# Kernel optimization log

Hardware: AMD Instinct MI355X
Metric: run time of the kernel (lower is better)

## Reference

```python
import jax, jax.numpy as jnp
from jax import lax
import numpy as np


def _conv1d(x, w, b):
    # x: (N, C, L), w: (O, I, K), stride 2, padding 1 -> matches nn.Conv1d(k=4, s=2, p=1)
    y = lax.conv_general_dilated(x, w, window_strides=(2,), padding=[(1, 1)],
                                 dimension_numbers=('NCH', 'OIH', 'NCH'))
    return y + b[None, :, None]


def setup_inputs() -> dict:
    key = jax.random.key(0)
    k = jax.random.split(key, 6)
    B, C_in, T = 32, 256, 2048
    H, D, K_codes = 1024, 512, 1024
    s = 0.02
    return {
        'x': jax.random.normal(k[0], (B, C_in, T), dtype=jnp.float32),
        'w1': jax.random.normal(k[1], (H, C_in, 4), dtype=jnp.float32) * s,
        'b1': jnp.zeros((H,), dtype=jnp.float32),
        'w2': jax.random.normal(k[2], (D, H, 4), dtype=jnp.float32) * s,
        'b2': jnp.zeros((D,), dtype=jnp.float32),
        'codebook': jax.random.normal(k[3], (K_codes, D), dtype=jnp.float32) * s,
    }


def reference(x, w1, b1, w2, b2, codebook):
    z_e = _conv1d(jax.nn.relu(_conv1d(x, w1, b1)), w2, b2)  # (B, D, T/4)
    B, D, T = z_e.shape
    flat = z_e.transpose(0, 2, 1).reshape(-1, D)  # (B*T, D)
    # squared Euclidean distance; argmin identical to cdist(p=2) argmin
    d2 = (jnp.sum(flat * flat, axis=1, keepdims=True)
          - 2.0 * flat @ codebook.T
          + jnp.sum(codebook * codebook, axis=1)[None, :])  # (B*T, K)
    encoding_indices = jnp.argmin(d2, axis=1)  # (B*T,)
    # NOTE: faithful to the original .view(z_e.shape) (a raw reshape, no permute back)
    z_q = codebook[encoding_indices].reshape(B, D, T)
    return (z_q, encoding_indices, z_e)
```

## Files before the change

### kernel.cpp

```cpp
#include <hip/hip_runtime.h>
#include <hip/hip_bf16.h>

using f16x8 = __attribute__((ext_vector_type(8))) _Float16;
using f32x4 = __attribute__((ext_vector_type(4))) float;

union PackU { unsigned u; _Float16 h[2]; };

__device__ inline unsigned split_pack(float v) {
    _Float16 h0 = (_Float16)v;
    float r = (v - (float)h0) * 4096.0f;
    PackU p; p.h[0] = h0; p.h[1] = (_Float16)r;
    return p.u;
}

__global__ __launch_bounds__(256) void split_kernel(const float* __restrict__ src,
                                                    unsigned* __restrict__ dst, int n4) {
    int g = blockIdx.x * 256 + threadIdx.x;
    if (g >= n4) return;
    float4 v = reinterpret_cast<const float4*>(src)[g];
    uint4 o;
    o.x = split_pack(v.x); o.y = split_pack(v.y);
    o.z = split_pack(v.z); o.w = split_pack(v.w);
    reinterpret_cast<uint4*>(dst)[g] = o;
}

#define BMt 128
#define BNt 128
#define BKt 32

__global__ __launch_bounds__(256, 2) void mfma_gemm(
    const unsigned* __restrict__ Ap, const unsigned* __restrict__ Bp,
    const float* __restrict__ bias,
    unsigned* __restrict__ OutP, float* __restrict__ OutF,
    int M, int N, int KK, int Cc, int L, int Lout, int LoutSh,
    int gatherMode, int mode)
{
    __shared__ uint4 As4[2][BMt * 8];
    __shared__ uint4 Bs4[2][BNt * 8];

    const int tid = threadIdx.x;
    const int m0 = blockIdx.y * BMt;
    const int n0 = blockIdx.x * BNt;

    const int srow = tid >> 1;
    const int kh = tid & 1;
    const int sw_s = srow & 7;
    const int am = m0 + srow;
    const int ab = am >> LoutSh;
    const int at = am & (Lout - 1);
    const unsigned* aprow = Ap + (size_t)ab * Cc * L;
    const int ai0 = 2 * at - 1;
    const unsigned* adir = Ap + (size_t)am * KK;
    const unsigned* brow = Bp + (size_t)(n0 + srow) * KK;

    const int lane = tid & 63;
    const int wv = tid >> 6;
    const int wr = wv >> 1, wc = wv & 1;
    const int l15 = lane & 15, lq = lane >> 4;

    f32x4 acc0[4][4] = {{{0.f}}};
    f32x4 acc1[4][4] = {{{0.f}}};

    uint4 pa[4], pb[4];

    auto loadT = [&](int k0) {
        if (gatherMode) {
            int cbase = (k0 >> 2) + kh * 4;
#pragma unroll
            for (int cl = 0; cl < 4; cl++) {
                const unsigned* base = aprow + (size_t)(cbase + cl) * L;
                unsigned q0 = 0, q3 = 0;
                if (ai0 >= 0) q0 = base[ai0];
                unsigned q1 = base[ai0 + 1];
                unsigned q2 = base[ai0 + 2];
                if (ai0 + 3 < L) q3 = base[ai0 + 3];
                pa[cl].x = q0; pa[cl].y = q1; pa[cl].z = q2; pa[cl].w = q3;
            }
        } else {
            const uint4* s = reinterpret_cast<const uint4*>(adir + k0 + kh * 16);
            pa[0] = s[0]; pa[1] = s[1]; pa[2] = s[2]; pa[3] = s[3];
        }
        const uint4* s = reinterpret_cast<const uint4*>(brow + k0 + kh * 16);
        pb[0] = s[0]; pb[1] = s[1]; pb[2] = s[2]; pb[3] = s[3];
    };

    auto stage = [&](int buf) {
#pragma unroll
        for (int ch = 0; ch < 2; ch++) {
            uint4 w0, w1, v0, v1;
            unsigned* W0 = (unsigned*)&w0; unsigned* W1 = (unsigned*)&w1;
            unsigned* V0 = (unsigned*)&v0; unsigned* V1 = (unsigned*)&v1;
#pragma unroll
            for (int j = 0; j < 4; j++) {
                int e0 = ch * 8 + 2 * j, e1 = e0 + 1;
                unsigned lo = ((const unsigned*)&pa[e0 >> 2])[e0 & 3];
                unsigned hi = ((const unsigned*)&pa[e1 >> 2])[e1 & 3];
                W0[j] = __builtin_amdgcn_perm(hi, lo, 0x05040100u);
                W1[j] = __builtin_amdgcn_perm(hi, lo, 0x07060302u);
                lo = ((const unsigned*)&pb[e0 >> 2])[e0 & 3];
                hi = ((const unsigned*)&pb[e1 >> 2])[e1 & 3];
                V0[j] = __builtin_amdgcn_perm(hi, lo, 0x05040100u);
                V1[j] = __builtin_amdgcn_perm(hi, lo, 0x07060302u);
            }
            int kc = kh * 2 + ch;
            As4[buf][srow * 8 + ((kc) ^ sw_s)] = w0;
            As4[buf][srow * 8 + ((4 + kc) ^ sw_s)] = w1;
            Bs4[buf][srow * 8 + ((kc) ^ sw_s)] = v0;
            Bs4[buf][srow * 8 + ((4 + kc) ^ sw_s)] = v1;
        }
    };

    const int NT = KK / BKt;

    loadT(0);
    stage(0);

    for (int kt = 0; kt < NT; kt++) {
        const int cur = kt & 1;
        if (kt + 1 < NT) loadT((kt + 1) * BKt);

        asm volatile("s_waitcnt lgkmcnt(0)\n\ts_barrier" ::: "memory");
        __builtin_amdgcn_sched_barrier(0);

        f16x8 a0f[4], a1f[4];
#pragma unroll
        for (int mf = 0; mf < 4; mf++) {
            int row = wr * 64 + mf * 16 + l15;
            int sw = row & 7;
            a0f[mf] = *reinterpret_cast<const f16x8*>(&As4[cur][row * 8 + (lq ^ sw)]);
            a1f[mf] = *reinterpret_cast<const f16x8*>(&As4[cur][row * 8 + ((4 + lq) ^ sw)]);
        }
#pragma unroll
        for (int nf = 0; nf < 4; nf++) {
            int row = wc * 64 + nf * 16 + l15;
            int sw = row & 7;
            f16x8 b0f = *reinterpret_cast<const f16x8*>(&Bs4[cur][row * 8 + (lq ^ sw)]);
            f16x8 b1f = *reinterpret_cast<const f16x8*>(&Bs4[cur][row * 8 + ((4 + lq) ^ sw)]);
#pragma unroll
            for (int mf = 0; mf < 4; mf++) {
                acc0[mf][nf] = __builtin_amdgcn_mfma_f32_16x16x32_f16(
                    a0f[mf], b0f, acc0[mf][nf], 0, 0, 0);
                acc1[mf][nf] = __builtin_amdgcn_mfma_f32_16x16x32_f16(
                    a0f[mf], b1f, acc1[mf][nf], 0, 0, 0);
                acc1[mf][nf] = __builtin_amdgcn_mfma_f32_16x16x32_f16(
                    a1f[mf], b0f, acc1[mf][nf], 0, 0, 0);
            }
        }

        if (kt + 1 < NT) stage(cur ^ 1);
    }

    const float s12 = 1.0f / 4096.0f;
    const int LoutM = Lout - 1;

    if (mode == 2) {
#pragma unroll
        for (int mf = 0; mf < 4; mf++) {
            int mb = m0 + wr * 64 + mf * 16 + lq * 4;
#pragma unroll
            for (int nf = 0; nf < 4; nf++) {
                int n = n0 + wc * 64 + nf * 16 + l15;
#pragma unroll
                for (int r = 0; r < 4; r++) {
                    float v = acc0[mf][nf][r] + acc1[mf][nf][r] * s12;
                    OutF[(size_t)(mb + r) * N + n] = v;
                }
            }
        }
    } else if (mode == 0) {
#pragma unroll
        for (int mf = 0; mf < 4; mf++) {
            int mb = m0 + wr * 64 + mf * 16 + lq * 4;
            int b = mb >> LoutSh, t = mb & LoutM;
#pragma unroll
            for (int nf = 0; nf < 4; nf++) {
                int n = n0 + wc * 64 + nf * 16 + l15;
                float bv = bias[n];
                uint4 o;
                unsigned* O = (unsigned*)&o;
#pragma unroll
                for (int r = 0; r < 4; r++) {
                    float v = acc0[mf][nf][r] + acc1[mf][nf][r] * s12 + bv;
                    v = fmaxf(v, 0.f);
                    O[r] = split_pack(v);
                }
                *reinterpret_cast<uint4*>(&OutP[((size_t)b * N + n) * Lout + t]) = o;
            }
        }
    } else {
#pragma unroll
        for (int mf = 0; mf < 4; mf++) {
            int mb = m0 + wr * 64 + mf * 16 + lq * 4;
            int b = mb >> LoutSh, t = mb & LoutM;
#pragma unroll
            for (int nf = 0; nf < 4; nf++) {
                int n = n0 + wc * 64 + nf * 16 + l15;
                float bv = bias[n];
                float4 f;
                unsigned O[4];
#pragma unroll
                for (int r = 0; r < 4; r++) {
                    float v = acc0[mf][nf][r] + acc1[mf][nf][r] * s12 + bv;
                    ((float*)&f)[r] = v;
                    O[r] = split_pack(v);
                }
                *reinterpret_cast<float4*>(&OutF[((size_t)b * N + n) * Lout + t]) = f;
#pragma unroll
                for (int r = 0; r < 4; r++)
                    OutP[(size_t)(mb + r) * N + n] = O[r];
            }
        }
    }
}

__global__ __launch_bounds__(64) void cb_norm(const float* __restrict__ cb,
                                              float* __restrict__ cn2) {
    int n = blockIdx.x;
    int lane = threadIdx.x;
    float s = 0.f;
    for (int d = lane; d < 512; d += 64) {
        float v = cb[(size_t)n * 512 + d];
        s += v * v;
    }
#pragma unroll
    for (int off = 32; off; off >>= 1) s += __shfl_down(s, off);
    if (lane == 0) cn2[n] = s;
}

__global__ __launch_bounds__(256) void argmin_k(const float* __restrict__ S,
                                                const float* __restrict__ cn2,
                                                float* __restrict__ idxf,
                                                int* __restrict__ idxi, int rows) {
    int wid = threadIdx.x >> 6;
    int lane = threadIdx.x & 63;
    int r = blockIdx.x * 4 + wid;
    if (r >= rows) return;
    const float* srow = S + (size_t)r * 1024;
    float best = INFINITY;
    int bi = 0;
#pragma unroll
    for (int it = 0; it < 4; it++) {
        int nb = it * 256 + lane * 4;
        float4 s4 = *reinterpret_cast<const float4*>(&srow[nb]);
        float4 c4 = *reinterpret_cast<const float4*>(&cn2[nb]);
        float v;
        v = c4.x - 2.f * s4.x; if (v < best) { best = v; bi = nb + 0; }
        v = c4.y - 2.f * s4.y; if (v < best) { best = v; bi = nb + 1; }
        v = c4.z - 2.f * s4.z; if (v < best) { best = v; bi = nb + 2; }
        v = c4.w - 2.f * s4.w; if (v < best) { best = v; bi = nb + 3; }
    }
#pragma unroll
    for (int off = 32; off; off >>= 1) {
        float ov = __shfl_down(best, off);
        int oi = __shfl_down(bi, off);
        if (ov < best || (ov == best && oi < bi)) { best = ov; bi = oi; }
    }
    if (lane == 0) {
        idxf[r] = (float)bi;
        idxi[r] = bi;
    }
}

__global__ __launch_bounds__(256) void gather_k(const int* __restrict__ idx,
                                                const float* __restrict__ cb,
                                                float* __restrict__ zq, int total4) {
    int g = blockIdx.x * 256 + threadIdx.x;
    if (g >= total4) return;
    int r = g >> 7;
    int d4 = g & 127;
    int id = idx[r];
    *reinterpret_cast<float4*>(&zq[(size_t)r * 512 + (size_t)d4 * 4]) =
        *reinterpret_cast<const float4*>(&cb[(size_t)id * 512 + (size_t)d4 * 4]);
}

extern "C" void kernel_launch(void* const* d_in, const int* in_sizes, int n_in,
                              void* d_out, int out_size, void* d_ws, size_t ws_size,
                              hipStream_t stream) {
    const float* x  = (const float*)d_in[0];
    const float* w1 = (const float*)d_in[1];
    const float* b1 = (const float*)d_in[2];
    const float* w2 = (const float*)d_in[3];
    const float* b2 = (const float*)d_in[4];
    const float* cb = (const float*)d_in[5];
    float* out = (float*)d_out;

    const int B = 32, Cin = 256, T = 2048, H = 1024, D = 512, Kc = 1024;
    const int T1 = 1024, T2 = 512;

    float* zq_out  = out;
    float* idx_out = out + (size_t)B * T2 * D;
    float* ze_out  = idx_out + (size_t)B * T2;

    unsigned* w1p = (unsigned*)d_ws;
    unsigned* w2p = w1p + (size_t)H * Cin * 4;
    unsigned* cbp = w2p + (size_t)D * H * 4;
    float* cn2    = (float*)(cbp + (size_t)Kc * D);
    int* idx_ws   = (int*)(cn2 + Kc);
    unsigned* dyn = (unsigned*)(idx_ws + B * T2);

    size_t fixed_u32 = (size_t)H * Cin * 4 + (size_t)D * H * 4 + (size_t)Kc * D
                       + Kc + (size_t)B * T2 + 256;
    int NB = 32;
    while (NB > 1 &&
           (fixed_u32 + (size_t)NB * ((size_t)Cin * T + (size_t)H * T1 + (size_t)T2 * D))
               * 4 > ws_size)
        NB >>= 1;

    unsigned* xp = dyn;
    unsigned* hp = xp + (size_t)NB * Cin * T;
    unsigned* zp = hp + (size_t)NB * H * T1;
    float* S = (float*)hp;

    split_kernel<<<(H * Cin * 4 / 4 + 255) / 256, 256, 0, stream>>>(w1, w1p, H * Cin * 4 / 4);
    split_kernel<<<(D * H * 4 / 4 + 255) / 256, 256, 0, stream>>>(w2, w2p, D * H * 4 / 4);
    split_kernel<<<(Kc * D / 4 + 255) / 256, 256, 0, stream>>>(cb, cbp, Kc * D / 4);
    cb_norm<<<Kc, 64, 0, stream>>>(cb, cn2);

    for (int b0 = 0; b0 < B; b0 += NB) {
        int nb = (B - b0 < NB) ? (B - b0) : NB;

        split_kernel<<<(nb * Cin * T / 4 + 255) / 256, 256, 0, stream>>>(
            x + (size_t)b0 * Cin * T, xp, nb * Cin * T / 4);

        mfma_gemm<<<dim3(H / BNt, nb * T1 / BMt), 256, 0, stream>>>(
            xp, w1p, b1, hp, nullptr,
            nb * T1, H, Cin * 4, Cin, T, T1, 10, 1, 0);

        mfma_gemm<<<dim3(D / BNt, nb * T2 / BMt), 256, 0, stream>>>(
            hp, w2p, b2, zp, ze_out + (size_t)b0 * D * T2,
            nb * T2, D, H * 4, H, T1, T2, 9, 1, 1);

        mfma_gemm<<<dim3(Kc / BNt, nb * T2 / BMt), 256, 0, stream>>>(
            zp, cbp, nullptr, nullptr, S,
            nb * T2, Kc, D, D, T2, T2, 9, 0, 2);

        argmin_k<<<(nb * T2 + 3) / 4, 256, 0, stream>>>(
            S, cn2, idx_out + (size_t)b0 * T2, idx_ws, nb * T2);

        gather_k<<<(nb * T2 * D / 4 + 255) / 256, 256, 0, stream>>>(
            idx_ws, cb, zq_out + (size_t)b0 * T2 * D, nb * T2 * D / 4);
    }
}
```

Before: 578.7 us.

## Pre-tile weight operands and stream them into LDS with direct global loads

Weights and codebook are now split and packed into the exact swizzled per-tile LDS layout ahead of time. The GEMM then copies its B tiles with global_load_lds straight into shared memory, skipping the register staging and perm shuffles. Manual vmcnt waits order these async copies against the A register loads, and s_setprio raises wave priority around the MFMA block. This cuts VGPR pressure and B-side instruction overhead, but the hand-written vmcnt counts must exactly match the outstanding loads or the kernel will read stale data.

```diff
diff --git a/kernel.cpp b/kernel.cpp
--- a/kernel.cpp
+++ b/kernel.cpp
@@ -11,6 +11,12 @@
     float r = (v - (float)h0) * 4096.0f;
     PackU p; p.h[0] = h0; p.h[1] = (_Float16)r;
     return p.u;
+}
+
+__device__ __forceinline__ void gll16(const uint4* g, uint4* l) {
+    __builtin_amdgcn_global_load_lds(
+        (const __attribute__((address_space(1))) uint4*)g,
+        (__attribute__((address_space(3))) uint4*)l, 16, 0, 0);
 }
 
 __global__ __launch_bounds__(256) void split_kernel(const float* __restrict__ src,
@@ -24,15 +30,39 @@
     reinterpret_cast<uint4*>(dst)[g] = o;
 }
 
+__global__ __launch_bounds__(256) void bsplit_gll(const float* __restrict__ src,
+        uint4* __restrict__ dst, int KK, int nTilesK, int total) {
+    int tid = blockIdx.x * 256 + threadIdx.x;
+    if (tid >= total) return;
+    int w = tid & 1023;
+    int tile = tid >> 10;
+    int kstep = tile % nTilesK;
+    int npanel = tile / nTilesK;
+    int r = w >> 3, c = w & 7;
+    int cp = c ^ (r & 7);
+    int p = cp >> 2, kg = cp & 3;
+    int n = npanel * 128 + r;
+    int k = kstep * 32 + kg * 8;
+    const float* s = src + (size_t)n * KK + k;
+    uint4 o;
+    ushort* h = (ushort*)&o;
+#pragma unroll
+    for (int j = 0; j < 8; j++) {
+        unsigned u = split_pack(s[j]);
+        h[j] = p ? (ushort)(u >> 16) : (ushort)u;
+    }
+    dst[tid] = o;
+}
+
 #define BMt 128
 #define BNt 128
 #define BKt 32
 
 __global__ __launch_bounds__(256, 2) void mfma_gemm(
-    const unsigned* __restrict__ Ap, const unsigned* __restrict__ Bp,
+    const unsigned* __restrict__ Ap, const uint4* __restrict__ Bg,
     const float* __restrict__ bias,
     unsigned* __restrict__ OutP, float* __restrict__ OutF,
-    int M, int N, int KK, int Cc, int L, int Lout, int LoutSh,
+    int M, int N, int KK, int nTilesK, int Cc, int L, int Lout, int LoutSh,
     int gatherMode, int mode)
 {
     __shared__ uint4 As4[2][BMt * 8];
@@ -51,17 +81,18 @@
     const unsigned* aprow = Ap + (size_t)ab * Cc * L;
     const int ai0 = 2 * at - 1;
     const unsigned* adir = Ap + (size_t)am * KK;
-    const unsigned* brow = Bp + (size_t)(n0 + srow) * KK;
 
     const int lane = tid & 63;
     const int wv = tid >> 6;
     const int wr = wv >> 1, wc = wv & 1;
     const int l15 = lane & 15, lq = lane >> 4;
 
+    const uint4* bsrc = Bg + (size_t)blockIdx.x * nTilesK * 1024;
+
     f32x4 acc0[4][4] = {{{0.f}}};
     f32x4 acc1[4][4] = {{{0.f}}};
 
-    uint4 pa[4], pb[4];
+    uint4 pa[4];
 
     auto loadT = [&](int k0) {
         if (gatherMode) {
@@ -78,18 +109,16 @@
             }
         } else {
             const uint4* s = reinterpret_cast<const uint4*>(adir + k0 + kh * 16);
-            pa[0] = s[0]; pa[1] = s[1]; pa[2] = s[2]; pa[3] = s[3];
-        }
-        const uint4* s = reinterpret_cast<const uint4*>(brow + k0 + kh * 16);
-        pb[0] = s[0]; pb[1] = s[1]; pb[2] = s[2]; pb[3] = s[3];
+#pragma unroll
+            for (int q = 0; q < 4; q++) pa[q] = s[q];
+        }
     };
 
     auto stage = [&](int buf) {
 #pragma unroll
         for (int ch = 0; ch < 2; ch++) {
-            uint4 w0, w1, v0, v1;
+            uint4 w0, w1;
             unsigned* W0 = (unsigned*)&w0; unsigned* W1 = (unsigned*)&w1;
-            unsigned* V0 = (unsigned*)&v0; unsigned* V1 = (unsigned*)&v1;
 #pragma unroll
             for (int j = 0; j < 4; j++) {
                 int e0 = ch * 8 + 2 * j, e1 = e0 + 1;
@@ -97,30 +126,40 @@
                 unsigned hi = ((const unsigned*)&pa[e1 >> 2])[e1 & 3];
                 W0[j] = __builtin_amdgcn_perm(hi, lo, 0x05040100u);
                 W1[j] = __builtin_amdgcn_perm(hi, lo, 0x07060302u);
-                lo = ((const unsigned*)&pb[e0 >> 2])[e0 & 3];
-                hi = ((const unsigned*)&pb[e1 >> 2])[e1 & 3];
-                V0[j] = __builtin_amdgcn_perm(hi, lo, 0x05040100u);
-                V1[j] = __builtin_amdgcn_perm(hi, lo, 0x07060302u);
             }
             int kc = kh * 2 + ch;
             As4[buf][srow * 8 + ((kc) ^ sw_s)] = w0;
             As4[buf][srow * 8 + ((4 + kc) ^ sw_s)] = w1;
-            Bs4[buf][srow * 8 + ((kc) ^ sw_s)] = v0;
-            Bs4[buf][srow * 8 + ((4 + kc) ^ sw_s)] = v1;
         }
     };
 
+    auto gllB = [&](int buf, int kt2) {
+        const uint4* ts = bsrc + (size_t)kt2 * 1024 + wv * 256 + lane;
+#pragma unroll
+        for (int i = 0; i < 4; i++)
+            gll16(ts + i * 64, &Bs4[buf][wv * 256 + i * 64]);
+    };
+
     const int NT = KK / BKt;
 
     loadT(0);
+    gllB(0, 0);
     stage(0);
 
     for (int kt = 0; kt < NT; kt++) {
         const int cur = kt & 1;
         if (kt + 1 < NT) loadT((kt + 1) * BKt);
 
+        if (kt + 1 < NT) {
+            if (gatherMode) asm volatile("s_waitcnt vmcnt(16)" ::: "memory");
+            else            asm volatile("s_waitcnt vmcnt(4)" ::: "memory");
+        } else {
+            asm volatile("s_waitcnt vmcnt(0)" ::: "memory");
+        }
         asm volatile("s_waitcnt lgkmcnt(0)\n\ts_barrier" ::: "memory");
         __builtin_amdgcn_sched_barrier(0);
+
+        if (kt + 1 < NT) gllB(cur ^ 1, kt + 1);
 
         f16x8 a0f[4], a1f[4];
 #pragma unroll
@@ -130,6 +169,7 @@
             a0f[mf] = *reinterpret_cast<const f16x8*>(&As4[cur][row * 8 + (lq ^ sw)]);
             a1f[mf] = *reinterpret_cast<const f16x8*>(&As4[cur][row * 8 + ((4 + lq) ^ sw)]);
         }
+        __builtin_amdgcn_s_setprio(1);
 #pragma unroll
         for (int nf = 0; nf < 4; nf++) {
             int row = wc * 64 + nf * 16 + l15;
@@ -146,6 +186,7 @@
                     a1f[mf], b0f, acc1[mf][nf], 0, 0, 0);
             }
         }
+        __builtin_amdgcn_s_setprio(0);
 
         if (kt + 1 < NT) stage(cur ^ 1);
     }
@@ -291,10 +332,10 @@
     float* idx_out = out + (size_t)B * T2 * D;
     float* ze_out  = idx_out + (size_t)B * T2;
 
-    unsigned* w1p = (unsigned*)d_ws;
-    unsigned* w2p = w1p + (size_t)H * Cin * 4;
-    unsigned* cbp = w2p + (size_t)D * H * 4;
-    float* cn2    = (float*)(cbp + (size_t)Kc * D);
+    unsigned* w1f = (unsigned*)d_ws;
+    unsigned* w2f = w1f + (size_t)H * Cin * 4;
+    unsigned* cbf = w2f + (size_t)D * H * 4;
+    float* cn2    = (float*)(cbf + (size_t)Kc * D);
     int* idx_ws   = (int*)(cn2 + Kc);
     unsigned* dyn = (unsigned*)(idx_ws + B * T2);
 
@@ -311,9 +352,12 @@
     unsigned* zp = hp + (size_t)NB * H * T1;
     float* S = (float*)hp;
 
-    split_kernel<<<(H * Cin * 4 / 4 + 255) / 256, 256, 0, stream>>>(w1, w1p, H * Cin * 4 / 4);
-    split_kernel<<<(D * H * 4 / 4 + 255) / 256, 256, 0, stream>>>(w2, w2p, D * H * 4 / 4);
-    split_kernel<<<(Kc * D / 4 + 255) / 256, 256, 0, stream>>>(cb, cbp, Kc * D / 4);
+    bsplit_gll<<<(H * (Cin * 4) / 4 + 255) / 256, 256, 0, stream>>>(
+        w1, (uint4*)w1f, Cin * 4, (Cin * 4) / 32, H * (Cin * 4) / 4);
+    bsplit_gll<<<(D * (H * 4) / 4 + 255) / 256, 256, 0, stream>>>(
+        w2, (uint4*)w2f, H * 4, (H * 4) / 32, D * (H * 4) / 4);
+    bsplit_gll<<<(Kc * D / 4 + 255) / 256, 256, 0, stream>>>(
+        cb, (uint4*)cbf, D, D / 32, Kc * D / 4);
     cb_norm<<<Kc, 64, 0, stream>>>(cb, cn2);
 
     for (int b0 = 0; b0 < B; b0 += NB) {
@@ -323,16 +367,16 @@
             x + (size_t)b0 * Cin * T, xp, nb * Cin * T / 4);
 
         mfma_gemm<<<dim3(H / BNt, nb * T1 / BMt), 256, 0, stream>>>(
-            xp, w1p, b1, hp, nullptr,
-            nb * T1, H, Cin * 4, Cin, T, T1, 10, 1, 0);
+            xp, (const uint4*)w1f, b1, hp, nullptr,
+            nb * T1, H, Cin * 4, (Cin * 4) / 32, Cin, T, T1, 10, 1, 0);
 
         mfma_gemm<<<dim3(D / BNt, nb * T2 / BMt), 256, 0, stream>>>(
-            hp, w2p, b2, zp, ze_out + (size_t)b0 * D * T2,
-            nb * T2, D, H * 4, H, T1, T2, 9, 1, 1);
+            hp, (const uint4*)w2f, b2, zp, ze_out + (size_t)b0 * D * T2,
+            nb * T2, D, H * 4, (H * 4) / 32, H, T1, T2, 9, 1, 1);
 
         mfma_gemm<<<dim3(Kc / BNt, nb * T2 / BMt), 256, 0, stream>>>(
-            zp, cbp, nullptr, nullptr, S,
-            nb * T2, Kc, D, D, T2, T2, 9, 0, 2);
+            zp, (const uint4*)cbf, nullptr, nullptr, S,
+            nb * T2, Kc, D, D / 32, D, T2, T2, 9, 0, 2);
 
         argmin_k<<<(nb * T2 + 3) / 4, 256, 0, stream>>>(
             S, cn2, idx_out + (size_t)b0 * T2, idx_ws, nb * T2);
```

Measured after the change: 579.2 us. No clear change (+0.1%).
